# Performance work log

Measured on AMD Instinct MI355X. Metric: run time of the kernel, lower is better.

Reference implementation:

```python
import jax, jax.numpy as jnp
import numpy as np
jax.config.update("jax_enable_x64", True)  # circuit computes internally in FP64

N = 4_194_304  # batch of scalar tanh evaluations
_SHIFTS = jnp.arange(31, -1, -1, dtype=jnp.uint32)  # MSB-first bit order, per make_fp64_constant


def f32_to_bits(v):
    """float32 [...,] -> [..., 32] 0/1 float32 pulses, MSB first."""
    u = jax.lax.bitcast_convert_type(v.astype(jnp.float32), jnp.uint32)
    return ((u[..., None] >> _SHIFTS) & jnp.uint32(1)).astype(jnp.float32)


def bits_to_f32(bits):
    """[..., 32] 0/1 pulses (MSB first) -> float32 [...]."""
    u = jnp.sum(bits.astype(jnp.uint32) << _SHIFTS, axis=-1, dtype=jnp.uint32)
    return jax.lax.bitcast_convert_type(u, jnp.float32)


def setup_inputs() -> dict:
    key = jax.random.key(0)
    vals = (jax.random.normal(key, (N,), dtype=jnp.float32) * 2.0).astype(jnp.float32)
    x = f32_to_bits(vals)  # [N, 32] valid IEEE-754 bit pulses
    return {"x": x}


def reference(x) -> jnp.ndarray:
    # The SNN circuit: FP32 bits -> FP64, then tanh(v) = (e^{2v} - 1) / (e^{2v} + 1)
    # entirely in FP64 arithmetic, then round back to FP32 bits.
    v64 = bits_to_f32(x).astype(jnp.float64)          # FP32ToFP64Converter
    e2x = jnp.exp(jnp.float64(2.0) * v64)             # fp64_mul + fp64_exp
    t64 = (e2x - 1.0) / (e2x + 1.0)                   # fp64_adder x2 + fp64_divider
    return f32_to_bits(t64.astype(jnp.float32))       # FP64ToFP32Converter -> [N, 32] pulses
```

## Files before the change

### kernel.cpp

```cpp
#include <hip/hip_runtime.h>

typedef unsigned int uint32;

__global__ __launch_bounds__(256) void
spike_tanh_kernel(const uint4* __restrict__ in, uint4* __restrict__ out, int n_elems) {
    const int stride = gridDim.x * blockDim.x;
    for (int i = blockIdx.x * blockDim.x + threadIdx.x; i < n_elems; i += stride) {
        const uint4* p = in + (size_t)i * 8;
        uint32 u = 0u;
#pragma unroll
        for (int k = 0; k < 8; ++k) {
            uint4 b = p[k];
            u = (u << 4) | ((b.x ? 8u : 0u) | (b.y ? 4u : 0u) |
                            (b.z ? 2u : 0u) | (b.w ? 1u : 0u));
        }
        float v;
        __builtin_memcpy(&v, &u, 4);

        double e2x = exp(2.0 * (double)v);
        double t64 = (e2x - 1.0) / (e2x + 1.0);
        float r = (float)t64;

        uint32 ru;
        __builtin_memcpy(&ru, &r, 4);

        uint4* q = out + (size_t)i * 8;
#pragma unroll
        for (int k = 0; k < 8; ++k) {
            uint4 o;
            o.x = (ru & 0x80000000u) ? 0x3F800000u : 0u;
            o.y = (ru & 0x40000000u) ? 0x3F800000u : 0u;
            o.z = (ru & 0x20000000u) ? 0x3F800000u : 0u;
            o.w = (ru & 0x10000000u) ? 0x3F800000u : 0u;
            ru <<= 4;
            q[k] = o;
        }
    }
}

extern "C" void kernel_launch(void* const* d_in, const int* in_sizes, int n_in,
                              void* d_out, int out_size, void* d_ws, size_t ws_size,
                              hipStream_t stream) {
    (void)n_in; (void)d_ws; (void)ws_size; (void)out_size;
    const int n_elems = in_sizes[0] / 32;
    const uint4* in  = (const uint4*)d_in[0];
    uint4*       out = (uint4*)d_out;

    const int block = 256;
    int grid = (n_elems + block - 1) / block;
    if (grid > 2048) grid = 2048;
    spike_tanh_kernel<<<grid, block, 0, stream>>>(in, out, n_elems);
}
```

Before: 892.6 us.

## Assign one uint4 per thread and assemble bit words via lane shuffles

Each thread now loads and stores a single 16-byte uint4 at consecutive addresses, so global memory accesses across the wavefront are fully coalesced. Previously each thread read and wrote 128 contiguous bytes, giving strided access. Groups of eight lanes combine their nibbles into the full 32-bit word with xor shuffles. The cost is that every lane computes the same FP64 exp and divide, so FP64 work grows eightfold.

```diff
diff --git a/kernel.cpp b/kernel.cpp
--- a/kernel.cpp
+++ b/kernel.cpp
@@ -3,38 +3,34 @@
 typedef unsigned int uint32;
 
 __global__ __launch_bounds__(256) void
-spike_tanh_kernel(const uint4* __restrict__ in, uint4* __restrict__ out, int n_elems) {
-    const int stride = gridDim.x * blockDim.x;
-    for (int i = blockIdx.x * blockDim.x + threadIdx.x; i < n_elems; i += stride) {
-        const uint4* p = in + (size_t)i * 8;
-        uint32 u = 0u;
-#pragma unroll
-        for (int k = 0; k < 8; ++k) {
-            uint4 b = p[k];
-            u = (u << 4) | ((b.x ? 8u : 0u) | (b.y ? 4u : 0u) |
-                            (b.z ? 2u : 0u) | (b.w ? 1u : 0u));
-        }
-        float v;
-        __builtin_memcpy(&v, &u, 4);
+spike_tanh_kernel(const uint4* __restrict__ in, uint4* __restrict__ out, long n_vec4) {
+    const long stride = (long)gridDim.x * blockDim.x;
+    const int pos   = threadIdx.x & 7;
+    const int shift = 4 * (7 - pos);
 
+    for (long i = (long)blockIdx.x * blockDim.x + threadIdx.x; i < n_vec4; i += stride) {
+        uint4 b = in[i];
+        uint32 nib = (b.x ? 8u : 0u) | (b.y ? 4u : 0u) |
+                     (b.z ? 2u : 0u) | (b.w ? 1u : 0u);
+        uint32 u = nib << shift;
+
+        u |= __shfl_xor(u, 1);
+        u |= __shfl_xor(u, 2);
+        u |= __shfl_xor(u, 4);
+
+        float v = __uint_as_float(u);
         double e2x = exp(2.0 * (double)v);
         double t64 = (e2x - 1.0) / (e2x + 1.0);
         float r = (float)t64;
+        uint32 ru = __float_as_uint(r);
 
-        uint32 ru;
-        __builtin_memcpy(&ru, &r, 4);
-
-        uint4* q = out + (size_t)i * 8;
-#pragma unroll
-        for (int k = 0; k < 8; ++k) {
-            uint4 o;
-            o.x = (ru & 0x80000000u) ? 0x3F800000u : 0u;
-            o.y = (ru & 0x40000000u) ? 0x3F800000u : 0u;
-            o.z = (ru & 0x20000000u) ? 0x3F800000u : 0u;
-            o.w = (ru & 0x10000000u) ? 0x3F800000u : 0u;
-            ru <<= 4;
-            q[k] = o;
-        }
+        uint32 onib = (ru >> shift) & 0xFu;
+        uint4 o;
+        o.x = (onib & 8u) ? 0x3F800000u : 0u;
+        o.y = (onib & 4u) ? 0x3F800000u : 0u;
+        o.z = (onib & 2u) ? 0x3F800000u : 0u;
+        o.w = (onib & 1u) ? 0x3F800000u : 0u;
+        out[i] = o;
     }
 }
 
@@ -42,12 +38,12 @@
                               void* d_out, int out_size, void* d_ws, size_t ws_size,
                               hipStream_t stream) {
     (void)n_in; (void)d_ws; (void)ws_size; (void)out_size;
-    const int n_elems = in_sizes[0] / 32;
+    const long n_vec4 = (long)in_sizes[0] / 4;
     const uint4* in  = (const uint4*)d_in[0];
     uint4*       out = (uint4*)d_out;
 
     const int block = 256;
-    int grid = (n_elems + block - 1) / block;
-    if (grid > 2048) grid = 2048;
-    spike_tanh_kernel<<<grid, block, 0, stream>>>(in, out, n_elems);
+    long grid_l = (n_vec4 + block - 1) / block;
+    int grid = grid_l > 2048 ? 2048 : (int)grid_l;
+    spike_tanh_kernel<<<grid, block, 0, stream>>>(in, out, n_vec4);
 }
```

Measured after the change: 844.7 us. -5.4%, faster.
